# Kernel optimization log

Measured on AMD Instinct MI355X. Metric: run time of the kernel, lower is better.

The kernel has to match this reference:

```python
import jax, jax.numpy as jnp
import numpy as np

PE_DIM = 40  # pe_dim; gaussian PE scale factor = pe_dim // 2


def _batched_linear(x, wb):
    # x: [B, N, D], wb: [B, D+1, H] (last row is bias)
    return jnp.einsum('bnd,bdh->bnh', x, wb[:, :-1, :]) + wb[:, -1:, :]


def setup_inputs() -> dict:
    key = jax.random.key(0)
    ks = jax.random.split(key, 8)
    B, N = 16, 16384
    H = 256
    pe_out = 3 * PE_DIM  # 120
    s = 0.05  # keep ReLU-chain activations bounded
    return {
        'x': jax.random.normal(ks[0], (B, N, 3), dtype=jnp.float32),
        'wb0': jax.random.normal(ks[1], (B, pe_out + 1, H), dtype=jnp.float32) * s,
        'wb1': jax.random.normal(ks[2], (B, H + 1, H), dtype=jnp.float32) * s,
        'wb2': jax.random.normal(ks[3], (B, H + 1, H), dtype=jnp.float32) * s,
        'wb3': jax.random.normal(ks[4], (B, H + 1, H), dtype=jnp.float32) * s,
        'wb4': jax.random.normal(ks[5], (B, H + 1, H), dtype=jnp.float32) * s,
        'wb_out': jax.random.normal(ks[6], (B, H + 1, 1), dtype=jnp.float32) * s,
        'rand_freqs': jax.random.normal(ks[7], (3 * (PE_DIM // 2), 3), dtype=jnp.float32),  # feat_sigma=1
    }


def reference(x, wb0, wb1, wb2, wb3, wb4, wb_out, rand_freqs):
    # Gaussian positional encoding: k = x . (rand_freqs * pe_dim//2)
    k = jnp.einsum('bnd,fd->bnf', x, rand_freqs * (PE_DIM // 2))  # [B,N,60]
    h = jnp.concatenate([jnp.sin(k), jnp.cos(k)], axis=-1)        # [B,N,120]
    for wb in (wb0, wb1, wb2, wb3, wb4):
        h = jax.nn.relu(_batched_linear(h, wb))
    out = _batched_linear(h, wb_out)  # [B,N,1]
    return out
```

## Files before the change

kernel.cpp:

```cpp
#include <hip/hip_runtime.h>
#include <hip/hip_bf16.h>


#define H 256
#define MT 128
#define PE_NF 60

typedef __attribute__((ext_vector_type(8))) short s16x8;
typedef __attribute__((ext_vector_type(4))) float f32x4;

static __device__ __forceinline__ unsigned short f2bf(float v) {
  unsigned int u = __float_as_uint(v);
  return (unsigned short)((u + 0x7FFFu + ((u >> 16) & 1u)) >> 16);
}
static __device__ __forceinline__ float bf2f(unsigned short u) {
  return __uint_as_float(((unsigned int)u) << 16);
}
static __device__ __forceinline__ int hswz(int row, int chunk) {
  return (chunk & ~7) | ((chunk ^ row) & 7);
}

static __device__ __forceinline__ void bar_raw() {
  asm volatile("s_barrier" ::: "memory");
}
static __device__ __forceinline__ void bar_lgkm() {
  asm volatile("s_waitcnt lgkmcnt(0)\n\ts_barrier" ::: "memory");
}

__global__ __launch_bounds__(256) void prep_weights(
    const float* __restrict__ wb0, const float* __restrict__ wb1,
    const float* __restrict__ wb2, const float* __restrict__ wb3,
    const float* __restrict__ wb4,
    unsigned short* __restrict__ w0p, unsigned short* __restrict__ w14p,
    float* __restrict__ biases) {
  int z = blockIdx.z;
  int li = z >> 4, b = z & 15;
  int k0 = blockIdx.x * 32;
  int n0 = blockIdx.y * 32;
  int Ks;
  const float* src;
  unsigned short* dst;
  if (li == 0) {
    Ks = 120;
    if (k0 >= 128) return;
    src = wb0 + (size_t)b * 121 * H;
    dst = w0p + (size_t)b * 32768;
  } else {
    Ks = 256;
    const float* srcs[4] = {wb1, wb2, wb3, wb4};
    src = srcs[li - 1] + (size_t)b * 257 * H;
    dst = w14p + ((size_t)(li - 1) * 16 + b) * 65536;
  }
  __shared__ float tile[32][33];
  int t = threadIdx.x;
  int tx = t & 31, ty = t >> 5;
#pragma unroll
  for (int i = 0; i < 4; ++i) {
    int k = k0 + ty + i * 8;
    tile[ty + i * 8][tx] = (k < Ks) ? src[(size_t)k * H + n0 + tx] : 0.f;
  }
  if (k0 == 0 && ty == 0)
    biases[((size_t)li * 16 + b) * H + n0 + tx] = src[(size_t)Ks * H + n0 + tx];
  __syncthreads();
  if (t < 128) {
    int nn = t & 31, kg = t >> 5;
    int n = n0 + nn;
    int kt = k0 >> 5;
    int w = n >> 6, ct = (n >> 4) & 3, rl = n & 15;
    union { unsigned short us[8]; s16x8 v; } pk;
#pragma unroll
    for (int j = 0; j < 8; ++j) pk.us[j] = f2bf(tile[kg * 8 + j][nn]);
    *(s16x8*)&dst[(size_t)(kt * 16 + w * 4 + ct) * 512 + (kg * 16 + rl) * 8] = pk.v;
  }
}

template <int NKT, bool LAST>
static __device__ __forceinline__ void mlp_layer(
    const unsigned short* __restrict__ wl, const unsigned short* __restrict__ wln,
    const float* __restrict__ bl, unsigned short* __restrict__ h_s,
    const int rlane, const int kgrp, const int w, const int l,
    s16x8 (&bb)[2][4]) {
  static_assert((NKT & 1) == 0, "ping-pong parity needs even NKT");
  const int n_base = w * 64;

  f32x4 acc[8][4];
  {
    f32x4 bini[4];
#pragma unroll
    for (int ct = 0; ct < 4; ++ct)
      bini[ct] = *(const f32x4*)(bl + n_base + ct * 16 + kgrp * 4);
#pragma unroll
    for (int rt = 0; rt < 8; ++rt)
#pragma unroll
      for (int ct = 0; ct < 4; ++ct) acc[rt][ct] = bini[ct];
  }

  const unsigned short* fp = wl + (size_t)(w * 4) * 512 + l * 8;
  int aoff[8];
#pragma unroll
  for (int rt = 0; rt < 8; ++rt) aoff[rt] = (rt * 16 + rlane) * 256;

#pragma unroll
  for (int kt = 0; kt < NKT; ++kt) {
    if (kt + 1 < NKT) {
#pragma unroll
      for (int ct = 0; ct < 4; ++ct)
        bb[(kt + 1) & 1][ct] = *(const s16x8*)(fp + (kt + 1) * 8192 + ct * 512);
    } else if (!LAST) {
      const unsigned short* fpn = wln + (size_t)(w * 4) * 512 + l * 8;
#pragma unroll
      for (int ct = 0; ct < 4; ++ct)
        bb[0][ct] = *(const s16x8*)(fpn + ct * 512);
    }
    s16x8 afr[8];
    const int cs = hswz(rlane, kt * 4 + kgrp) * 8;
#pragma unroll
    for (int rt = 0; rt < 8; ++rt)
      afr[rt] = *(const s16x8*)&h_s[aoff[rt] + cs];
    __builtin_amdgcn_s_setprio(1);
#pragma unroll
    for (int rt = 0; rt < 8; ++rt)
#pragma unroll
      for (int ct = 0; ct < 4; ++ct)
        acc[rt][ct] = __builtin_amdgcn_mfma_f32_16x16x32_bf16(
            bb[kt & 1][ct], afr[rt], acc[rt][ct], 0, 0, 0);
    __builtin_amdgcn_s_setprio(0);
  }
  bar_raw();

  const int sub = (kgrp & 1) * 4;
  const int cbase = w * 8 + (kgrp >> 1);
#pragma unroll
  for (int rt = 0; rt < 8; ++rt) {
    const int m = rt * 16 + rlane;
    const int rowb = m * 256;
#pragma unroll
    for (int ct = 0; ct < 4; ++ct) {
      const int cs = hswz(m, cbase + ct * 2);
      float v0 = fmaxf(acc[rt][ct][0], 0.f);
      float v1 = fmaxf(acc[rt][ct][1], 0.f);
      float v2 = fmaxf(acc[rt][ct][2], 0.f);
      float v3 = fmaxf(acc[rt][ct][3], 0.f);
      union { __hip_bfloat162 h2[2]; uint2 u; } pk;
      pk.h2[0] = __float22bfloat162_rn(float2{v0, v1});
      pk.h2[1] = __float22bfloat162_rn(float2{v2, v3});
      *(uint2*)&h_s[rowb + cs * 8 + sub] = pk.u;
    }
  }
  bar_lgkm();
}

__global__ __launch_bounds__(256, 2) void hyponerf_main(
    const float* __restrict__ x, const float* __restrict__ rfreq,
    const float* __restrict__ wbout,
    const unsigned short* __restrict__ w0p, const unsigned short* __restrict__ w14p,
    const float* __restrict__ biases, float* __restrict__ out) {
  __shared__ __align__(16) unsigned short h_s[MT * 256];
  __shared__ float fr_s[PE_NF * 3];
  __shared__ float x_s[MT * 3];
  __shared__ float wout_s[H + 1];

  int bid = blockIdx.x;
  int logical = (bid & 7) * 256 + (bid >> 3);
  int b  = logical >> 7;
  int mt = logical & 127;

  int t = threadIdx.x;
  int w = t >> 6, l = t & 63;
  int rlane = l & 15;
  int kgrp  = l >> 4;

  const unsigned short* wl0 = w0p + (size_t)b * 32768;
  const unsigned short* wl1 = w14p + (size_t)(0 * 16 + b) * 65536;
  const unsigned short* wl2 = w14p + (size_t)(1 * 16 + b) * 65536;
  const unsigned short* wl3 = w14p + (size_t)(2 * 16 + b) * 65536;
  const unsigned short* wl4 = w14p + (size_t)(3 * 16 + b) * 65536;

  s16x8 bb[2][4];
  {
    const unsigned short* fp0 = wl0 + (size_t)(w * 4) * 512 + l * 8;
#pragma unroll
    for (int ct = 0; ct < 4; ++ct) bb[0][ct] = *(const s16x8*)(fp0 + ct * 512);
  }

  const float* xg = x + ((size_t)b * 16384 + (size_t)mt * MT) * 3;
  for (int i = t; i < MT * 3; i += 256) x_s[i] = xg[i];
  for (int i = t; i < PE_NF * 3; i += 256) fr_s[i] = rfreq[i] * 20.0f;
  for (int i = t; i < H + 1; i += 256) wout_s[i] = wbout[(size_t)b * (H + 1) + i];
  bar_lgkm();

  {
    int r = t >> 1;
    int q = t & 1;
    float x0 = x_s[r * 3 + 0], x1 = x_s[r * 3 + 1], x2 = x_s[r * 3 + 2];
    int rowb = r * 256;
#pragma unroll
    for (int cc = 0; cc < 8; ++cc) {
      union { unsigned short us[8]; s16x8 v; } pk;
#pragma unroll
      for (int j = 0; j < 8; ++j) {
        int n = q * 64 + cc * 8 + j;
        float v = 0.f;
        if (n < 60) {
          float kv = x0 * fr_s[n * 3] + x1 * fr_s[n * 3 + 1] + x2 * fr_s[n * 3 + 2];
          v = __sinf(kv);
        } else if (n < 120) {
          int f = n - 60;
          float kv = x0 * fr_s[f * 3] + x1 * fr_s[f * 3 + 1] + x2 * fr_s[f * 3 + 2];
          v = __cosf(kv);
        }
        pk.us[j] = f2bf(v);
      }
      *(s16x8*)&h_s[rowb + hswz(r, q * 8 + cc) * 8] = pk.v;
    }
  }
  bar_lgkm();

  mlp_layer<4, false>(wl0, wl1, biases + (size_t)(0 * 16 + b) * H, h_s,
                      rlane, kgrp, w, l, bb);
  mlp_layer<8, false>(wl1, wl2, biases + (size_t)(1 * 16 + b) * H, h_s,
                      rlane, kgrp, w, l, bb);
  mlp_layer<8, false>(wl2, wl3, biases + (size_t)(2 * 16 + b) * H, h_s,
                      rlane, kgrp, w, l, bb);
  mlp_layer<8, false>(wl3, wl4, biases + (size_t)(3 * 16 + b) * H, h_s,
                      rlane, kgrp, w, l, bb);
  mlp_layer<8, true >(wl4, wl4, biases + (size_t)(4 * 16 + b) * H, h_s,
                      rlane, kgrp, w, l, bb);

  {
    int r = t >> 1;
    int cb = (t & 1) * 16;
    int rowb = r * 256;
    float sum = 0.f;
#pragma unroll
    for (int c = 0; c < 16; ++c) {
      int ch = cb + c;
      const s16x8 hv = *(const s16x8*)&h_s[rowb + hswz(r, ch) * 8];
#pragma unroll
      for (int j = 0; j < 8; ++j)
        sum += bf2f((unsigned short)hv[j]) * wout_s[ch * 8 + j];
    }
    sum += __shfl_xor(sum, 1);
    if ((t & 1) == 0)
      out[(size_t)b * 16384 + (size_t)mt * MT + r] = sum + wout_s[H];
  }
}

extern "C" void kernel_launch(void* const* d_in, const int* in_sizes, int n_in,
                              void* d_out, int out_size, void* d_ws, size_t ws_size,
                              hipStream_t stream) {
  const float* x     = (const float*)d_in[0];
  const float* wb0   = (const float*)d_in[1];
  const float* wb1   = (const float*)d_in[2];
  const float* wb2   = (const float*)d_in[3];
  const float* wb3   = (const float*)d_in[4];
  const float* wb4   = (const float*)d_in[5];
  const float* wbout = (const float*)d_in[6];
  const float* rfreq = (const float*)d_in[7];
  float* out = (float*)d_out;

  char* ws = (char*)d_ws;
  unsigned short* w0p  = (unsigned short*)ws;
  unsigned short* w14p = (unsigned short*)(ws + (size_t)16 * 32768 * 2);
  float* biases = (float*)(ws + (size_t)16 * 32768 * 2
                              + (size_t)64 * 65536 * 2);

  prep_weights<<<dim3(8, 8, 80), 256, 0, stream>>>(wb0, wb1, wb2, wb3, wb4,
                                                   w0p, w14p, biases);
  hyponerf_main<<<dim3(2048), 256, 0, stream>>>(x, rfreq, wbout, w0p, w14p,
                                                biases, out);
}
```

Baseline: 174.6 us.

## Tile waves 2x2 over rows and columns with split weight-fragment pipelining

After: 204.6 us. 17.2% more time.

```diff
diff --git a/kernel.cpp b/kernel.cpp
--- a/kernel.cpp
+++ b/kernel.cpp
@@ -66,11 +66,10 @@
     int nn = t & 31, kg = t >> 5;
     int n = n0 + nn;
     int kt = k0 >> 5;
-    int w = n >> 6, ct = (n >> 4) & 3, rl = n & 15;
     union { unsigned short us[8]; s16x8 v; } pk;
 #pragma unroll
     for (int j = 0; j < 8; ++j) pk.us[j] = f2bf(tile[kg * 8 + j][nn]);
-    *(s16x8*)&dst[(size_t)(kt * 16 + w * 4 + ct) * 512 + (kg * 16 + rl) * 8] = pk.v;
+    *(s16x8*)&dst[(size_t)(kt * 16 + (n >> 4)) * 512 + (kg * 16 + (n & 15)) * 8] = pk.v;
   }
 }
 
@@ -78,64 +77,73 @@
 static __device__ __forceinline__ void mlp_layer(
     const unsigned short* __restrict__ wl, const unsigned short* __restrict__ wln,
     const float* __restrict__ bl, unsigned short* __restrict__ h_s,
-    const int rlane, const int kgrp, const int w, const int l,
-    s16x8 (&bb)[2][4]) {
-  static_assert((NKT & 1) == 0, "ping-pong parity needs even NKT");
-  const int n_base = w * 64;
-
-  f32x4 acc[8][4];
-  {
-    f32x4 bini[4];
-#pragma unroll
-    for (int ct = 0; ct < 4; ++ct)
-      bini[ct] = *(const f32x4*)(bl + n_base + ct * 16 + kgrp * 4);
-#pragma unroll
-    for (int rt = 0; rt < 8; ++rt)
-#pragma unroll
-      for (int ct = 0; ct < 4; ++ct) acc[rt][ct] = bini[ct];
-  }
-
-  const unsigned short* fp = wl + (size_t)(w * 4) * 512 + l * 8;
-  int aoff[8];
-#pragma unroll
-  for (int rt = 0; rt < 8; ++rt) aoff[rt] = (rt * 16 + rlane) * 256;
+    const int rlane, const int kgrp, const int wr, const int wc, const int l,
+    s16x8 (&wfA)[4]) {
+  f32x4 acc[4][8];
+#pragma unroll
+  for (int ct = 0; ct < 8; ++ct) {
+    f32x4 bini = *(const f32x4*)(bl + wc * 128 + ct * 16 + kgrp * 4);
+#pragma unroll
+    for (int rt = 0; rt < 4; ++rt) acc[rt][ct] = bini;
+  }
+
+  const unsigned short* fp = wl + (size_t)(wc * 8) * 512 + l * 8;
+  int aoff[4];
+#pragma unroll
+  for (int rt = 0; rt < 4; ++rt) aoff[rt] = (wr * 64 + rt * 16 + rlane) * 256;
+
+  s16x8 af[2][4];
+  {
+    const int cs = hswz(rlane, kgrp) * 8;
+#pragma unroll
+    for (int rt = 0; rt < 4; ++rt)
+      af[0][rt] = *(const s16x8*)&h_s[aoff[rt] + cs];
+  }
+  s16x8 wfB[4];
 
 #pragma unroll
   for (int kt = 0; kt < NKT; ++kt) {
+#pragma unroll
+    for (int c = 0; c < 4; ++c)
+      wfB[c] = *(const s16x8*)(fp + (kt * 16 + 4 + c) * 512);
+#pragma unroll
+    for (int rt = 0; rt < 4; ++rt)
+#pragma unroll
+      for (int c = 0; c < 4; ++c)
+        acc[rt][c] = __builtin_amdgcn_mfma_f32_16x16x32_bf16(
+            wfA[c], af[kt & 1][rt], acc[rt][c], 0, 0, 0);
+
     if (kt + 1 < NKT) {
 #pragma unroll
-      for (int ct = 0; ct < 4; ++ct)
-        bb[(kt + 1) & 1][ct] = *(const s16x8*)(fp + (kt + 1) * 8192 + ct * 512);
+      for (int c = 0; c < 4; ++c)
+        wfA[c] = *(const s16x8*)(fp + ((kt + 1) * 16 + c) * 512);
+      const int cs = hswz(rlane, (kt + 1) * 4 + kgrp) * 8;
+#pragma unroll
+      for (int rt = 0; rt < 4; ++rt)
+        af[(kt + 1) & 1][rt] = *(const s16x8*)&h_s[aoff[rt] + cs];
     } else if (!LAST) {
-      const unsigned short* fpn = wln + (size_t)(w * 4) * 512 + l * 8;
-#pragma unroll
-      for (int ct = 0; ct < 4; ++ct)
-        bb[0][ct] = *(const s16x8*)(fpn + ct * 512);
-    }
-    s16x8 afr[8];
-    const int cs = hswz(rlane, kt * 4 + kgrp) * 8;
-#pragma unroll
-    for (int rt = 0; rt < 8; ++rt)
-      afr[rt] = *(const s16x8*)&h_s[aoff[rt] + cs];
-    __builtin_amdgcn_s_setprio(1);
-#pragma unroll
-    for (int rt = 0; rt < 8; ++rt)
-#pragma unroll
-      for (int ct = 0; ct < 4; ++ct)
-        acc[rt][ct] = __builtin_amdgcn_mfma_f32_16x16x32_bf16(
-            bb[kt & 1][ct], afr[rt], acc[rt][ct], 0, 0, 0);
-    __builtin_amdgcn_s_setprio(0);
+      const unsigned short* fpn = wln + (size_t)(wc * 8) * 512 + l * 8;
+#pragma unroll
+      for (int c = 0; c < 4; ++c)
+        wfA[c] = *(const s16x8*)(fpn + c * 512);
+    }
+#pragma unroll
+    for (int rt = 0; rt < 4; ++rt)
+#pragma unroll
+      for (int c = 0; c < 4; ++c)
+        acc[rt][c + 4] = __builtin_amdgcn_mfma_f32_16x16x32_bf16(
+            wfB[c], af[kt & 1][rt], acc[rt][c + 4], 0, 0, 0);
   }
   bar_raw();
 
   const int sub = (kgrp & 1) * 4;
-  const int cbase = w * 8 + (kgrp >> 1);
-#pragma unroll
-  for (int rt = 0; rt < 8; ++rt) {
-    const int m = rt * 16 + rlane;
+  const int cbase = wc * 16 + (kgrp >> 1);
+#pragma unroll
+  for (int rt = 0; rt < 4; ++rt) {
+    const int m = wr * 64 + rt * 16 + rlane;
     const int rowb = m * 256;
 #pragma unroll
-    for (int ct = 0; ct < 4; ++ct) {
+    for (int ct = 0; ct < 8; ++ct) {
       const int cs = hswz(m, cbase + ct * 2);
       float v0 = fmaxf(acc[rt][ct][0], 0.f);
       float v1 = fmaxf(acc[rt][ct][1], 0.f);
@@ -169,6 +177,7 @@
   int w = t >> 6, l = t & 63;
   int rlane = l & 15;
   int kgrp  = l >> 4;
+  int wr = w >> 1, wc = w & 1;
 
   const unsigned short* wl0 = w0p + (size_t)b * 32768;
   const unsigned short* wl1 = w14p + (size_t)(0 * 16 + b) * 65536;
@@ -176,11 +185,11 @@
   const unsigned short* wl3 = w14p + (size_t)(2 * 16 + b) * 65536;
   const unsigned short* wl4 = w14p + (size_t)(3 * 16 + b) * 65536;
 
-  s16x8 bb[2][4];
-  {
-    const unsigned short* fp0 = wl0 + (size_t)(w * 4) * 512 + l * 8;
-#pragma unroll
-    for (int ct = 0; ct < 4; ++ct) bb[0][ct] = *(const s16x8*)(fp0 + ct * 512);
+  s16x8 wfA[4];
+  {
+    const unsigned short* fp0 = wl0 + (size_t)(wc * 8) * 512 + l * 8;
+#pragma unroll
+    for (int c = 0; c < 4; ++c) wfA[c] = *(const s16x8*)(fp0 + c * 512);
   }
 
   const float* xg = x + ((size_t)b * 16384 + (size_t)mt * MT) * 3;
@@ -217,15 +226,15 @@
   bar_lgkm();
 
   mlp_layer<4, false>(wl0, wl1, biases + (size_t)(0 * 16 + b) * H, h_s,
-                      rlane, kgrp, w, l, bb);
+                      rlane, kgrp, wr, wc, l, wfA);
   mlp_layer<8, false>(wl1, wl2, biases + (size_t)(1 * 16 + b) * H, h_s,
-                      rlane, kgrp, w, l, bb);
+                      rlane, kgrp, wr, wc, l, wfA);
   mlp_layer<8, false>(wl2, wl3, biases + (size_t)(2 * 16 + b) * H, h_s,
-                      rlane, kgrp, w, l, bb);
+                      rlane, kgrp, wr, wc, l, wfA);
   mlp_layer<8, false>(wl3, wl4, biases + (size_t)(3 * 16 + b) * H, h_s,
-                      rlane, kgrp, w, l, bb);
+                      rlane, kgrp, wr, wc, l, wfA);
   mlp_layer<8, true >(wl4, wl4, biases + (size_t)(4 * 16 + b) * H, h_s,
-                      rlane, kgrp, w, l, bb);
+                      rlane, kgrp, wr, wc, l, wfA);
 
   {
     int r = t >> 1;
```
